# Kernel optimization log

Hardware: AMD Instinct MI355X
Metric: run time of the kernel (lower is better)

The kernel has to match this reference:

```python
import jax, jax.numpy as jnp
import numpy as np

N_CHEM = 200000
N_GENE = 20000
N_EDGES = 1000000
IN, HID, OUT = 128, 256, 128


def _seg_mean(msg, dst, num_segments):
    # DGL fn.mean: mean of incoming messages; nodes with zero in-degree get 0.
    s = jax.ops.segment_sum(msg, dst, num_segments=num_segments)
    cnt = jax.ops.segment_sum(jnp.ones((msg.shape[0],), msg.dtype), dst,
                              num_segments=num_segments)[:, None]
    return jnp.where(cnt > 0, s / jnp.maximum(cnt, 1.0), 0.0)


def setup_inputs() -> dict:
    key = jax.random.key(0)
    ks = jax.random.split(key, 12)
    d = {
        'src_cg': jax.random.randint(ks[0], (N_EDGES,), 0, N_CHEM, dtype=jnp.int32),
        'dst_cg': jax.random.randint(ks[1], (N_EDGES,), 0, N_GENE, dtype=jnp.int32),
        'src_gc': jax.random.randint(ks[2], (N_EDGES,), 0, N_GENE, dtype=jnp.int32),
        'dst_gc': jax.random.randint(ks[3], (N_EDGES,), 0, N_CHEM, dtype=jnp.int32),
        'embed_chem': jax.random.normal(ks[4], (N_CHEM, IN), jnp.float32) * 0.1,
        'embed_gene': jax.random.normal(ks[5], (N_GENE, IN), jnp.float32) * 0.1,
        'W1_cg': jax.random.normal(ks[6], (IN, HID), jnp.float32) * (1.0 / np.sqrt(IN)),
        'b1_cg': jnp.zeros((HID,), jnp.float32),
        'W1_gc': jax.random.normal(ks[7], (IN, HID), jnp.float32) * (1.0 / np.sqrt(IN)),
        'b1_gc': jnp.zeros((HID,), jnp.float32),
        'W2_cg': jax.random.normal(ks[8], (HID, OUT), jnp.float32) * (1.0 / np.sqrt(HID)),
        'b2_cg': jnp.zeros((OUT,), jnp.float32),
        'W2_gc': jax.random.normal(ks[9], (HID, OUT), jnp.float32) * (1.0 / np.sqrt(HID)),
        'b2_gc': jnp.zeros((OUT,), jnp.float32),
    }
    return d


def _layer(h_chem, h_gene, W_cg, b_cg, W_gc, b_gc, src_cg, dst_cg, src_gc, dst_gc):
    # per-etype linear transform on source features
    Wh_cg = h_chem @ W_cg + b_cg   # [N_CHEM, D]
    Wh_gc = h_gene @ W_gc + b_gc   # [N_GENE, D]
    # copy_u + mean per etype; multi_update_all('sum') -> single etype per dst here
    new_gene = _seg_mean(Wh_cg[src_cg], dst_cg, N_GENE)
    new_chem = _seg_mean(Wh_gc[src_gc], dst_gc, N_CHEM)
    return new_chem, new_gene


def reference(src_cg, dst_cg, src_gc, dst_gc, embed_chem, embed_gene,
              W1_cg, b1_cg, W1_gc, b1_gc, W2_cg, b2_cg, W2_gc, b2_gc):
    h_chem, h_gene = _layer(embed_chem, embed_gene, W1_cg, b1_cg, W1_gc, b1_gc,
                            src_cg, dst_cg, src_gc, dst_gc)
    h_chem = jax.nn.leaky_relu(h_chem, negative_slope=0.01)
    h_gene = jax.nn.leaky_relu(h_gene, negative_slope=0.01)
    h_chem, _ = _layer(h_chem, h_gene, W2_cg, b2_cg, W2_gc, b2_gc,
                       src_cg, dst_cg, src_gc, dst_gc)
    return h_chem  # [N_CHEM, OUT]
```

## Files before the change

### kernel.cpp

```cpp
#include <hip/hip_runtime.h>
#include <stdint.h>
#include <stddef.h>

#define N_CHEM 200000
#define N_GENE 20000
#define N_EDGES 1000000
#define IN_D 128
#define HID_D 256
#define OUT_D 128
#define N_SEG (N_GENE + N_CHEM)

#define NGB 313
#define NCB 391
#define NB  (NGB + NCB)
#define EPB 4096
#define NBA ((2 * N_EDGES + EPB - 1) / EPB)
#define CAP 8192
#define DROPPED 0x80000000

typedef float nfloat4 __attribute__((ext_vector_type(4)));
typedef __attribute__((ext_vector_type(8))) short bf16x8;
typedef __attribute__((ext_vector_type(4))) float f32x4;

__device__ inline unsigned bf16rne(float x) {
    unsigned u = __float_as_uint(x);
    return (u + 0x7FFFu + ((u >> 16) & 1u)) >> 16;
}

__device__ inline int bucket_of(int slot) {
    return (slot < N_GENE) ? (slot >> 6) : (NGB + ((slot - N_GENE) >> 9));
}
__device__ inline int bucket_slot0(int b) {
    return (b < NGB) ? (b << 6) : (N_GENE + ((b - NGB) << 9));
}


__global__ __launch_bounds__(256) void place_convert_kernel(
        const int* __restrict__ src_cg, const int* __restrict__ dst_cg,
        const int* __restrict__ src_gc, const int* __restrict__ dst_gc,
        int* __restrict__ bcur, unsigned* __restrict__ records,
        const float* __restrict__ conv_in, unsigned short* __restrict__ conv_out) {
    if ((int)blockIdx.x >= NBA) {
        int cb = blockIdx.x - NBA;
        const int tid = threadIdx.x;
        #pragma unroll
        for (int q = 0; q < 4; ++q) {
            int i = cb * 1024 + q * 256 + tid;
            if (i < N_CHEM * IN_D / 4) {
                float4 v = *(const float4*)&conv_in[(size_t)i * 4];
                uint2 w;
                w.x = bf16rne(v.x) | (bf16rne(v.y) << 16);
                w.y = bf16rne(v.z) | (bf16rne(v.w) << 16);
                *(uint2*)&conv_out[(size_t)i * 4] = w;
            }
        }
        return;
    }
    __shared__ unsigned stage_rec[EPB];
    __shared__ unsigned short stage_bkt[EPB];
    __shared__ int hist[NB];
    __shared__ int cursor[NB];
    __shared__ int tsum[256];
    const int tid = threadIdx.x;
    const int e0 = blockIdx.x * EPB;
    const int cnt_blk = min(EPB, 2 * N_EDGES - e0);

    for (int i = tid; i < NB; i += 256) hist[i] = 0;
    __syncthreads();

    int slotR[EPB / 256], srcR[EPB / 256];
    #pragma unroll
    for (int q = 0; q < EPB / 256; ++q) {
        int e = e0 + q * 256 + tid;
        int slot = -1, s = 0;
        if (e < N_EDGES)            { slot = dst_cg[e];                    s = src_cg[e]; }
        else if (e < 2 * N_EDGES)   { slot = N_GENE + dst_gc[e - N_EDGES]; s = src_gc[e - N_EDGES]; }
        slotR[q] = slot; srcR[q] = s;
        if (slot >= 0) atomicAdd(&hist[bucket_of(slot)], 1);
    }
    __syncthreads();

    const int b3 = tid * 3;
    int h0 = (b3     < NB) ? hist[b3]     : 0;
    int h1 = (b3 + 1 < NB) ? hist[b3 + 1] : 0;
    int h2 = (b3 + 2 < NB) ? hist[b3 + 2] : 0;
    int ts = h0 + h1 + h2;
    tsum[tid] = ts;
    __syncthreads();
    for (int off = 1; off < 256; off <<= 1) {
        int t = (tid >= off) ? tsum[tid - off] : 0;
        __syncthreads();
        tsum[tid] += t;
        __syncthreads();
    }
    int base = tsum[tid] - ts;
    if (b3     < NB) cursor[b3]     = base;
    if (b3 + 1 < NB) cursor[b3 + 1] = base + h0;
    if (b3 + 2 < NB) cursor[b3 + 2] = base + h0 + h1;
    __syncthreads();

    #pragma unroll
    for (int q = 0; q < EPB / 256; ++q) {
        int slot = slotR[q];
        if (slot >= 0) {
            int b = bucket_of(slot);
            int p = atomicAdd(&cursor[b], 1);
            stage_rec[p] = ((unsigned)(slot - bucket_slot0(b)) << 18) | (unsigned)srcR[q];
            stage_bkt[p] = (unsigned short)b;
        }
    }
    __syncthreads();

    for (int i = tid; i < NB; i += 256) {
        int n = hist[i];
        if (n) {
            int got = atomicAdd(&bcur[i], n);
            int excl_i = cursor[i] - n;
            hist[i] = (got + n <= CAP) ? (i * CAP + got - excl_i) : (int)DROPPED;
        }
    }
    __syncthreads();

    for (int i = tid; i < cnt_blk; i += 256) {
        int d = hist[stage_bkt[i]];
        if (d != (int)DROPPED) records[i + d] = stage_rec[i];
    }
}


__global__ void bucket_scan_kernel(const int* __restrict__ bcur,
                                   int* __restrict__ bbase, int* __restrict__ indptr) {
    __shared__ int sm[1024];
    const int tid = threadIdx.x;
    int v = (tid < NB) ? min(bcur[tid], CAP) : 0;
    sm[tid] = v;
    __syncthreads();
    for (int off = 1; off < 1024; off <<= 1) {
        int t = (tid >= off) ? sm[tid - off] : 0;
        __syncthreads();
        sm[tid] += t;
        __syncthreads();
    }
    if (tid < NB) bbase[tid] = sm[tid] - v;
    if (tid == NB - 1) {
        bbase[NB] = sm[tid];
        indptr[N_SEG] = sm[tid];
    }
}


__global__ __launch_bounds__(256) void bin_b_kernel(
        const unsigned* __restrict__ records, const int* __restrict__ bbase,
        const int* __restrict__ bcur,
        int* __restrict__ indptr, int* __restrict__ esrc) {
    __shared__ int hist[512];
    __shared__ int tsum[256];
    const int tid = threadIdx.x;
    const int b = blockIdx.x;
    int slot0 = bucket_slot0(b);
    int nslots = (b < NGB) ? min(64, N_GENE - slot0) : min(512, N_SEG - slot0);
    const int rbase = bbase[b];
    const int E = min(bcur[b], CAP);
    const unsigned* rec = &records[(size_t)b * CAP];

    hist[tid] = 0; hist[tid + 256] = 0;
    __syncthreads();
    for (int i = tid; i < E; i += 256)
        atomicAdd(&hist[rec[i] >> 18], 1);
    __syncthreads();

    int h0 = hist[2 * tid], h1 = hist[2 * tid + 1];
    int ts = h0 + h1;
    tsum[tid] = ts;
    __syncthreads();
    for (int off = 1; off < 256; off <<= 1) {
        int t = (tid >= off) ? tsum[tid - off] : 0;
        __syncthreads();
        tsum[tid] += t;
        __syncthreads();
    }
    int ex = tsum[tid] - ts;
    __syncthreads();
    hist[2 * tid]     = ex;
    hist[2 * tid + 1] = ex + h0;
    if (2 * tid     < nslots) indptr[slot0 + 2 * tid]     = rbase + ex;
    if (2 * tid + 1 < nslots) indptr[slot0 + 2 * tid + 1] = rbase + ex + h0;
    __syncthreads();

    for (int i = tid; i < E; i += 256) {
        unsigned r = rec[i];
        int p = atomicAdd(&hist[r >> 18], 1);
        esrc[rbase + p] = (int)(r & 0x3FFFFu);
    }
}


__device__ inline void acc_u(float* a, uint4 v) {
    a[0] += __uint_as_float(v.x << 16); a[1] += __uint_as_float(v.x & 0xffff0000u);
    a[2] += __uint_as_float(v.y << 16); a[3] += __uint_as_float(v.y & 0xffff0000u);
    a[4] += __uint_as_float(v.z << 16); a[5] += __uint_as_float(v.z & 0xffff0000u);
    a[6] += __uint_as_float(v.w << 16); a[7] += __uint_as_float(v.w & 0xffff0000u);
}


__global__ __launch_bounds__(256) void gather_mean_bf16_split_kernel(
        const unsigned short* __restrict__ table,
        const int* __restrict__ indptr, const int* __restrict__ esrc,
        unsigned short* __restrict__ outb, int n) {
    int lane = threadIdx.x & 15;
    int half = (threadIdx.x >> 4) & 1;
    int node = blockIdx.x * 8 + (threadIdx.x >> 5);
    if (node >= n) return;
    int s = indptr[node], e = indptr[node + 1];
    int deg = e - s;
    int mid = s + ((deg + 1) >> 1);
    int j0 = half ? mid : s;
    int j1 = half ? e   : mid;
    int c = lane << 3;
    float acc[8] = {};
    int j = j0;
    for (; j + 8 <= j1; j += 8) {
        int i0 = esrc[j],     i1 = esrc[j + 1], i2 = esrc[j + 2], i3 = esrc[j + 3];
        int i4 = esrc[j + 4], i5 = esrc[j + 5], i6 = esrc[j + 6], i7 = esrc[j + 7];
        uint4 v0 = *(const uint4*)&table[(size_t)i0 * 128 + c];
        uint4 v1 = *(const uint4*)&table[(size_t)i1 * 128 + c];
        uint4 v2 = *(const uint4*)&table[(size_t)i2 * 128 + c];
        uint4 v3 = *(const uint4*)&table[(size_t)i3 * 128 + c];
        uint4 v4 = *(const uint4*)&table[(size_t)i4 * 128 + c];
        uint4 v5 = *(const uint4*)&table[(size_t)i5 * 128 + c];
        uint4 v6 = *(const uint4*)&table[(size_t)i6 * 128 + c];
        uint4 v7 = *(const uint4*)&table[(size_t)i7 * 128 + c];
        acc_u(acc, v0); acc_u(acc, v1); acc_u(acc, v2); acc_u(acc, v3);
        acc_u(acc, v4); acc_u(acc, v5); acc_u(acc, v6); acc_u(acc, v7);
    }
    for (; j + 4 <= j1; j += 4) {
        uint4 v0 = *(const uint4*)&table[(size_t)esrc[j]     * 128 + c];
        uint4 v1 = *(const uint4*)&table[(size_t)esrc[j + 1] * 128 + c];
        uint4 v2 = *(const uint4*)&table[(size_t)esrc[j + 2] * 128 + c];
        uint4 v3 = *(const uint4*)&table[(size_t)esrc[j + 3] * 128 + c];
        acc_u(acc, v0); acc_u(acc, v1); acc_u(acc, v2); acc_u(acc, v3);
    }
    for (; j < j1; ++j) {
        uint4 v = *(const uint4*)&table[(size_t)esrc[j] * 128 + c];
        acc_u(acc, v);
    }
    #pragma unroll
    for (int q = 0; q < 8; ++q) acc[q] += __shfl_xor(acc[q], 16);
    if (half == 0) {
        float inv = (deg > 0) ? 1.f / (float)deg : 0.f;
        #pragma unroll
        for (int q = 0; q < 8; ++q) acc[q] *= inv;
        uint4 w;
        w.x = bf16rne(acc[0]) | (bf16rne(acc[1]) << 16);
        w.y = bf16rne(acc[2]) | (bf16rne(acc[3]) << 16);
        w.z = bf16rne(acc[4]) | (bf16rne(acc[5]) << 16);
        w.w = bf16rne(acc[6]) | (bf16rne(acc[7]) << 16);
        *(uint4*)&outb[(size_t)node * 128 + c] = w;
    }
}


template<bool NT>
__global__ __launch_bounds__(256) void gather_mean_bf16_kernel(
        const unsigned short* __restrict__ table,
        const int* __restrict__ indptr, const int* __restrict__ esrc,
        float* __restrict__ out, int n) {
    int lane = threadIdx.x & 15;
    int node = blockIdx.x * 16 + (threadIdx.x >> 4);
    if (node >= n) return;
    int s = indptr[node], e = indptr[node + 1];
    int c = lane << 3;
    float acc[8] = {};
    int j = s;
    for (; j + 4 <= e; j += 4) {
        uint4 v0 = *(const uint4*)&table[(size_t)esrc[j]     * 128 + c];
        uint4 v1 = *(const uint4*)&table[(size_t)esrc[j + 1] * 128 + c];
        uint4 v2 = *(const uint4*)&table[(size_t)esrc[j + 2] * 128 + c];
        uint4 v3 = *(const uint4*)&table[(size_t)esrc[j + 3] * 128 + c];
        acc_u(acc, v0); acc_u(acc, v1); acc_u(acc, v2); acc_u(acc, v3);
    }
    for (; j < e; ++j) {
        uint4 v = *(const uint4*)&table[(size_t)esrc[j] * 128 + c];
        acc_u(acc, v);
    }
    int deg = e - s;
    float inv = (deg > 0) ? 1.f / (float)deg : 0.f;
    #pragma unroll
    for (int q = 0; q < 8; ++q) acc[q] *= inv;
    float* dst = &out[(size_t)node * 128 + c];
    if (NT) {
        nfloat4 a = { acc[0], acc[1], acc[2], acc[3] };
        nfloat4 b = { acc[4], acc[5], acc[6], acc[7] };
        __builtin_nontemporal_store(a, (nfloat4*)dst);
        __builtin_nontemporal_store(b, (nfloat4*)(dst + 4));
    } else {
        *(float4*)dst       = make_float4(acc[0], acc[1], acc[2], acc[3]);
        *(float4*)(dst + 4) = make_float4(acc[4], acc[5], acc[6], acc[7]);
    }
}


__global__ __launch_bounds__(256) void gather_mean_f32_kernel(
        const float* __restrict__ table,
        const int* __restrict__ indptr, const int* __restrict__ esrc,
        float* __restrict__ out, int n) {
    int lane = threadIdx.x & 31;
    int node = blockIdx.x * 8 + (threadIdx.x >> 5);
    if (node >= n) return;
    int s = indptr[node], e = indptr[node + 1];
    int c = lane << 2;
    float4 acc = make_float4(0.f, 0.f, 0.f, 0.f);
    int j = s;
    for (; j + 4 <= e; j += 4) {
        int s0 = esrc[j], s1 = esrc[j + 1], s2 = esrc[j + 2], s3 = esrc[j + 3];
        float4 v0 = *(const float4*)&table[(size_t)s0 * 128 + c];
        float4 v1 = *(const float4*)&table[(size_t)s1 * 128 + c];
        float4 v2 = *(const float4*)&table[(size_t)s2 * 128 + c];
        float4 v3 = *(const float4*)&table[(size_t)s3 * 128 + c];
        acc.x += (v0.x + v1.x) + (v2.x + v3.x);
        acc.y += (v0.y + v1.y) + (v2.y + v3.y);
        acc.z += (v0.z + v1.z) + (v2.z + v3.z);
        acc.w += (v0.w + v1.w) + (v2.w + v3.w);
    }
    for (; j < e; ++j) {
        float4 v = *(const float4*)&table[(size_t)esrc[j] * 128 + c];
        acc.x += v.x; acc.y += v.y; acc.z += v.z; acc.w += v.w;
    }
    int deg = e - s;
    float inv = (deg > 0) ? 1.f / (float)deg : 0.f;
    acc.x *= inv; acc.y *= inv; acc.z *= inv; acc.w *= inv;
    *(float4*)&out[(size_t)node * 128 + c] = acc;
}


template<int K, int N, bool MASK_LEAKY>
__global__ __launch_bounds__(256) void gemm_mfma_kernel(
        const unsigned short* __restrict__ A,
        const float* __restrict__ W,
        const float* __restrict__ bias,
        const int* __restrict__ indptr,
        unsigned short* __restrict__ C,
        int M) {
    constexpr int BK  = 128;
    constexpr int LDK = BK + 8;
    __shared__ unsigned short As[64 * LDK];
    __shared__ unsigned short Ws[64 * LDK];
    const int tid  = threadIdx.x;
    const int lane = tid & 63;
    const int w    = tid >> 6;
    const int m0 = blockIdx.x * 64;
    const int n0 = blockIdx.y * 64;
    const int l15 = lane & 15;
    const int lhi = lane >> 4;
    f32x4 acc[4] = {};

    for (int kt0 = 0; kt0 < K; kt0 += BK) {
        #pragma unroll
        for (int it = 0; it < 4; ++it) {
            int idx = it * 256 + tid;
            int row = idx >> 4;
            int c8  = (idx & 15) << 3;
            uint4 v = make_uint4(0u, 0u, 0u, 0u);
            if (m0 + row < M)
                v = *(const uint4*)&A[(size_t)(m0 + row) * K + kt0 + c8];
            *(uint4*)&As[row * LDK + c8] = v;
        }
        #pragma unroll
        for (int it = 0; it < 32; ++it) {
            int i = it * 256 + tid;
            int k = i >> 6;
            int n = i & 63;
            float f = W[(size_t)(kt0 + k) * N + n0 + n];
            Ws[n * LDK + k] = (unsigned short)bf16rne(f);
        }
        __syncthreads();

        #pragma unroll
        for (int kk = 0; kk < BK; kk += 32) {
            bf16x8 a = *(const bf16x8*)&As[(w * 16 + l15) * LDK + kk + lhi * 8];
            #pragma unroll
            for (int nt = 0; nt < 4; ++nt) {
                bf16x8 b = *(const bf16x8*)&Ws[(nt * 16 + l15) * LDK + kk + lhi * 8];
                acc[nt] = __builtin_amdgcn_mfma_f32_16x16x32_bf16(a, b, acc[nt], 0, 0, 0);
            }
        }
        __syncthreads();
    }

    #pragma unroll
    for (int nt = 0; nt < 4; ++nt) {
        int col = n0 + nt * 16 + l15;
        float bz = bias[col];
        #pragma unroll
        for (int r = 0; r < 4; ++r) {
            int row = m0 + w * 16 + lhi * 4 + r;
            if (row < M) {
                float v = acc[nt][r] + bz;
                if (MASK_LEAKY) {
                    int deg = indptr[row + 1] - indptr[row];
                    v = (deg == 0) ? 0.f : (v > 0.f ? v : 0.01f * v);
                }
                C[(size_t)row * N + col] = (unsigned short)bf16rne(v);
            }
        }
    }
}


template<int K, int N, bool MASK_LEAKY, bool BF16_OUT>
__global__ __launch_bounds__(256) void gemm_kernel(const float* __restrict__ A,
                                                   const float* __restrict__ W,
                                                   const float* __restrict__ bias,
                                                   const int* __restrict__ indptr,
                                                   void* __restrict__ Cout, int M) {
    __shared__ float As[64 * 68];
    __shared__ float Ws[64 * 64];
    const int tid = threadIdx.x;
    const int tx = tid & 15, ty = tid >> 4;
    const int m0 = blockIdx.x * 64;
    const int n0 = blockIdx.y * 64;
    const int r0 = ty << 2, c0 = tx << 2;
    float acc[4][4] = {};

    for (int kt = 0; kt < K; kt += 64) {
        #pragma unroll
        for (int q = 0; q < 4; ++q) {
            int idx = tid + q * 256;
            int row = idx >> 4;
            int c4  = (idx & 15) << 2;
            float4 v = make_float4(0.f, 0.f, 0.f, 0.f);
            if (m0 + row < M)
                v = *(const float4*)&A[(size_t)(m0 + row) * K + kt + c4];
            *(float4*)&As[row * 68 + c4] = v;
        }
        #pragma unroll
        for (int q = 0; q < 4; ++q) {
            int idx = tid + q * 256;
            int k   = idx >> 4;
            int c4  = (idx & 15) << 2;
            *(float4*)&Ws[(k << 6) + c4] =
                *(const float4*)&W[(size_t)(kt + k) * N + n0 + c4];
        }
        __syncthreads();

        #pragma unroll 4
        for (int k = 0; k < 64; k += 4) {
            float a[4][4];
            #pragma unroll
            for (int r = 0; r < 4; ++r) {
                float4 v = *(const float4*)&As[(r0 + r) * 68 + k];
                a[r][0] = v.x; a[r][1] = v.y; a[r][2] = v.z; a[r][3] = v.w;
            }
            #pragma unroll
            for (int kk = 0; kk < 4; ++kk) {
                float4 w = *(const float4*)&Ws[((k + kk) << 6) + c0];
                #pragma unroll
                for (int r = 0; r < 4; ++r) {
                    acc[r][0] = fmaf(a[r][kk], w.x, acc[r][0]);
                    acc[r][1] = fmaf(a[r][kk], w.y, acc[r][1]);
                    acc[r][2] = fmaf(a[r][kk], w.z, acc[r][2]);
                    acc[r][3] = fmaf(a[r][kk], w.w, acc[r][3]);
                }
            }
        }
        __syncthreads();
    }

    float4 b = *(const float4*)&bias[n0 + c0];
    #pragma unroll
    for (int r = 0; r < 4; ++r) {
        int row = m0 + r0 + r;
        if (row < M) {
            float4 v;
            v.x = acc[r][0] + b.x; v.y = acc[r][1] + b.y;
            v.z = acc[r][2] + b.z; v.w = acc[r][3] + b.w;
            if (MASK_LEAKY) {
                int deg = indptr[row + 1] - indptr[row];
                if (deg == 0) {
                    v = make_float4(0.f, 0.f, 0.f, 0.f);
                } else {
                    v.x = v.x > 0.f ? v.x : 0.01f * v.x;
                    v.y = v.y > 0.f ? v.y : 0.01f * v.y;
                    v.z = v.z > 0.f ? v.z : 0.01f * v.z;
                    v.w = v.w > 0.f ? v.w : 0.01f * v.w;
                }
            }
            if (BF16_OUT) {
                uint2 w;
                w.x = bf16rne(v.x) | (bf16rne(v.y) << 16);
                w.y = bf16rne(v.z) | (bf16rne(v.w) << 16);
                *(uint2*)&((unsigned short*)Cout)[(size_t)row * N + n0 + c0] = w;
            } else {
                *(float4*)&((float*)Cout)[(size_t)row * N + n0 + c0] = v;
            }
        }
    }
}


extern "C" void kernel_launch(void* const* d_in, const int* in_sizes, int n_in,
                              void* d_out, int out_size, void* d_ws, size_t ws_size,
                              hipStream_t stream) {
    const int*   src_cg     = (const int*)d_in[0];
    const int*   dst_cg     = (const int*)d_in[1];
    const int*   src_gc     = (const int*)d_in[2];
    const int*   dst_gc     = (const int*)d_in[3];
    const float* embed_chem = (const float*)d_in[4];
    const float* W1_cg = (const float*)d_in[6];
    const float* b1_cg = (const float*)d_in[7];
    const float* W2_gc = (const float*)d_in[12];
    const float* b2_gc = (const float*)d_in[13];
    float* out = (float*)d_out;

    int* ws_i = (int*)d_ws;
    size_t off = 0;
    int* bcur  = ws_i + off; off += NB;
    int* bbase = ws_i + off; off += NB + 1;
    off = (off + 3) & ~(size_t)3;
    int* indptr = ws_i + off; off += N_SEG + 1; off = (off + 3) & ~(size_t)3;
    int* esrc   = ws_i + off; off += 2 * N_EDGES;
    size_t union_off = off;
    unsigned* records = (unsigned*)(ws_i + union_off);
    unsigned short* agg1b   = (unsigned short*)(ws_i + union_off);
    unsigned short* h_geneb = agg1b + (size_t)N_GENE * IN_D;
    float* agg1f   = (float*)(ws_i + union_off);
    float* h_genef = agg1f + (size_t)N_GENE * IN_D;
    size_t union_sz = (size_t)N_GENE * (IN_D + HID_D);
    off = union_off + union_sz;
    unsigned short* Wh2b = (unsigned short*)(ws_i + off); off += (size_t)N_GENE * OUT_D / 2;
    unsigned short* embedb = (unsigned short*)(ws_i + off);
    size_t off_full = off + (size_t)N_CHEM * IN_D / 2;
    const bool bf16_embed = ws_size >= off_full * sizeof(int);

    (void)hipMemsetAsync(bcur, 0, NB * sizeof(int), stream);

    const int nconv = bf16_embed ? (N_CHEM * IN_D / 4 + 1023) / 1024 : 0;
    place_convert_kernel<<<NBA + nconv, 256, 0, stream>>>(
        src_cg, dst_cg, src_gc, dst_gc, bcur, records, embed_chem, embedb);
    bucket_scan_kernel<<<1, 1024, 0, stream>>>(bcur, bbase, indptr);
    bin_b_kernel<<<NB, 256, 0, stream>>>(records, bbase, bcur, indptr, esrc);

    if (bf16_embed) {
        gather_mean_bf16_split_kernel<<<(N_GENE + 7) / 8, 256, 0, stream>>>(
            embedb, indptr, esrc, agg1b, N_GENE);
        {
            dim3 g((N_GENE + 63) / 64, HID_D / 64), blk(256);
            gemm_mfma_kernel<IN_D, HID_D, true><<<g, blk, 0, stream>>>(
                agg1b, W1_cg, b1_cg, indptr, h_geneb, N_GENE);
        }
        {
            dim3 g((N_GENE + 63) / 64, OUT_D / 64), blk(256);
            gemm_mfma_kernel<HID_D, OUT_D, false><<<g, blk, 0, stream>>>(
                h_geneb, W2_gc, b2_gc, nullptr, Wh2b, N_GENE);
        }
    } else {
        gather_mean_f32_kernel<<<(N_GENE + 7) / 8, 256, 0, stream>>>(
            embed_chem, indptr, esrc, agg1f, N_GENE);
        {
            dim3 g((N_GENE + 63) / 64, HID_D / 64), blk(256);
            gemm_kernel<IN_D, HID_D, true, false><<<g, blk, 0, stream>>>(
                agg1f, W1_cg, b1_cg, indptr, h_genef, N_GENE);
        }
        {
            dim3 g((N_GENE + 63) / 64, OUT_D / 64), blk(256);
            gemm_kernel<HID_D, OUT_D, false, true><<<g, blk, 0, stream>>>(
                h_genef, W2_gc, b2_gc, nullptr, Wh2b, N_GENE);
        }
    }

    gather_mean_bf16_kernel<true><<<(N_CHEM + 15) / 16, 256, 0, stream>>>(
        Wh2b, indptr + N_GENE, esrc, out, N_CHEM);
}
```

Before: 378.0 us.

## Drop bucket scan via fixed-capacity CSR and fuse the two gene GEMMs

Removes the single-block bucket scan kernel by giving each bucket a fixed CAP-sized region of esrc and storing per-node start/end arrays instead of a compact indptr. It also fuses the layer-1 GEMM (with bias, degree mask and leaky ReLU) and the layer-2 GEMM into one kernel that keeps the 64x256 hidden tile in shared memory as bf16. This saves two kernel launches plus the global write and read of the hidden activations. In exchange, esrc becomes a larger sparse buffer, the workspace grows, and the fused kernel uses more LDS per block and launches only a 1D grid of row tiles, which lowers parallelism.

Measured after the change: 380.9 us. No clear change (+0.8%).

```diff
diff --git a/kernel.cpp b/kernel.cpp
--- a/kernel.cpp
+++ b/kernel.cpp
@@ -128,38 +128,16 @@
 }
 
 
-__global__ void bucket_scan_kernel(const int* __restrict__ bcur,
-                                   int* __restrict__ bbase, int* __restrict__ indptr) {
-    __shared__ int sm[1024];
-    const int tid = threadIdx.x;
-    int v = (tid < NB) ? min(bcur[tid], CAP) : 0;
-    sm[tid] = v;
-    __syncthreads();
-    for (int off = 1; off < 1024; off <<= 1) {
-        int t = (tid >= off) ? sm[tid - off] : 0;
-        __syncthreads();
-        sm[tid] += t;
-        __syncthreads();
-    }
-    if (tid < NB) bbase[tid] = sm[tid] - v;
-    if (tid == NB - 1) {
-        bbase[NB] = sm[tid];
-        indptr[N_SEG] = sm[tid];
-    }
-}
-
-
 __global__ __launch_bounds__(256) void bin_b_kernel(
-        const unsigned* __restrict__ records, const int* __restrict__ bbase,
-        const int* __restrict__ bcur,
-        int* __restrict__ indptr, int* __restrict__ esrc) {
+        const unsigned* __restrict__ records, const int* __restrict__ bcur,
+        int* __restrict__ istart, int* __restrict__ iend, int* __restrict__ esrc) {
     __shared__ int hist[512];
     __shared__ int tsum[256];
     const int tid = threadIdx.x;
     const int b = blockIdx.x;
     int slot0 = bucket_slot0(b);
     int nslots = (b < NGB) ? min(64, N_GENE - slot0) : min(512, N_SEG - slot0);
-    const int rbase = bbase[b];
+    const int rbase = b * CAP;
     const int E = min(bcur[b], CAP);
     const unsigned* rec = &records[(size_t)b * CAP];
 
@@ -183,8 +161,14 @@
     __syncthreads();
     hist[2 * tid]     = ex;
     hist[2 * tid + 1] = ex + h0;
-    if (2 * tid     < nslots) indptr[slot0 + 2 * tid]     = rbase + ex;
-    if (2 * tid + 1 < nslots) indptr[slot0 + 2 * tid + 1] = rbase + ex + h0;
+    if (2 * tid < nslots) {
+        istart[slot0 + 2 * tid] = rbase + ex;
+        iend[slot0 + 2 * tid]   = rbase + ex + h0;
+    }
+    if (2 * tid + 1 < nslots) {
+        istart[slot0 + 2 * tid + 1] = rbase + ex + h0;
+        iend[slot0 + 2 * tid + 1]   = rbase + ex + h0 + h1;
+    }
     __syncthreads();
 
     for (int i = tid; i < E; i += 256) {
@@ -205,13 +189,14 @@
 
 __global__ __launch_bounds__(256) void gather_mean_bf16_split_kernel(
         const unsigned short* __restrict__ table,
-        const int* __restrict__ indptr, const int* __restrict__ esrc,
+        const int* __restrict__ istart, const int* __restrict__ iend,
+        const int* __restrict__ esrc,
         unsigned short* __restrict__ outb, int n) {
     int lane = threadIdx.x & 15;
     int half = (threadIdx.x >> 4) & 1;
     int node = blockIdx.x * 8 + (threadIdx.x >> 5);
     if (node >= n) return;
-    int s = indptr[node], e = indptr[node + 1];
+    int s = istart[node], e = iend[node];
     int deg = e - s;
     int mid = s + ((deg + 1) >> 1);
     int j0 = half ? mid : s;
@@ -263,12 +248,13 @@
 template<bool NT>
 __global__ __launch_bounds__(256) void gather_mean_bf16_kernel(
         const unsigned short* __restrict__ table,
-        const int* __restrict__ indptr, const int* __restrict__ esrc,
+        const int* __restrict__ istart, const int* __restrict__ iend,
+        const int* __restrict__ esrc,
         float* __restrict__ out, int n) {
     int lane = threadIdx.x & 15;
     int node = blockIdx.x * 16 + (threadIdx.x >> 4);
     if (node >= n) return;
-    int s = indptr[node], e = indptr[node + 1];
+    int s = istart[node], e = iend[node];
     int c = lane << 3;
     float acc[8] = {};
     int j = s;
@@ -302,12 +288,13 @@
 
 __global__ __launch_bounds__(256) void gather_mean_f32_kernel(
         const float* __restrict__ table,
-        const int* __restrict__ indptr, const int* __restrict__ esrc,
+        const int* __restrict__ istart, const int* __restrict__ iend,
+        const int* __restrict__ esrc,
         float* __restrict__ out, int n) {
     int lane = threadIdx.x & 31;
     int node = blockIdx.x * 8 + (threadIdx.x >> 5);
     if (node >= n) return;
-    int s = indptr[node], e = indptr[node + 1];
+    int s = istart[node], e = iend[node];
     int c = lane << 2;
     float4 acc = make_float4(0.f, 0.f, 0.f, 0.f);
     int j = s;
@@ -333,50 +320,51 @@
 }
 
 
-template<int K, int N, bool MASK_LEAKY>
-__global__ __launch_bounds__(256) void gemm_mfma_kernel(
+__global__ __launch_bounds__(256) void gemm_fused_kernel(
         const unsigned short* __restrict__ A,
-        const float* __restrict__ W,
-        const float* __restrict__ bias,
-        const int* __restrict__ indptr,
+        const float* __restrict__ W1,
+        const float* __restrict__ b1,
+        const float* __restrict__ W2,
+        const float* __restrict__ b2,
+        const int* __restrict__ istart, const int* __restrict__ iend,
         unsigned short* __restrict__ C,
         int M) {
-    constexpr int BK  = 128;
-    constexpr int LDK = BK + 8;
-    __shared__ unsigned short As[64 * LDK];
-    __shared__ unsigned short Ws[64 * LDK];
+    constexpr int LDK = 136;
+    constexpr int LDH = 264;
+    __shared__ unsigned short SAB[2 * 64 * LDK];
+    __shared__ unsigned short Ht[64 * LDH];
+    unsigned short* As = SAB;
+    unsigned short* Ws = SAB + 64 * LDK;
     const int tid  = threadIdx.x;
     const int lane = tid & 63;
     const int w    = tid >> 6;
-    const int m0 = blockIdx.x * 64;
-    const int n0 = blockIdx.y * 64;
-    const int l15 = lane & 15;
-    const int lhi = lane >> 4;
-    f32x4 acc[4] = {};
-
-    for (int kt0 = 0; kt0 < K; kt0 += BK) {
-        #pragma unroll
-        for (int it = 0; it < 4; ++it) {
-            int idx = it * 256 + tid;
-            int row = idx >> 4;
-            int c8  = (idx & 15) << 3;
-            uint4 v = make_uint4(0u, 0u, 0u, 0u);
-            if (m0 + row < M)
-                v = *(const uint4*)&A[(size_t)(m0 + row) * K + kt0 + c8];
-            *(uint4*)&As[row * LDK + c8] = v;
-        }
+    const int m0   = blockIdx.x * 64;
+    const int l15  = lane & 15;
+    const int lhi  = lane >> 4;
+
+    #pragma unroll
+    for (int it = 0; it < 4; ++it) {
+        int idx = it * 256 + tid;
+        int row = idx >> 4;
+        int c8  = (idx & 15) << 3;
+        uint4 v = make_uint4(0u, 0u, 0u, 0u);
+        if (m0 + row < M)
+            v = *(const uint4*)&A[(size_t)(m0 + row) * IN_D + c8];
+        *(uint4*)&As[row * LDK + c8] = v;
+    }
+    for (int n0c = 0; n0c < HID_D; n0c += 64) {
+        __syncthreads();
         #pragma unroll
         for (int it = 0; it < 32; ++it) {
             int i = it * 256 + tid;
             int k = i >> 6;
             int n = i & 63;
-            float f = W[(size_t)(kt0 + k) * N + n0 + n];
-            Ws[n * LDK + k] = (unsigned short)bf16rne(f);
-        }
-        __syncthreads();
-
-        #pragma unroll
-        for (int kk = 0; kk < BK; kk += 32) {
+            Ws[n * LDK + k] = (unsigned short)bf16rne(W1[(size_t)k * HID_D + n0c + n]);
+        }
+        __syncthreads();
+        f32x4 acc[4] = {};
+        #pragma unroll
+        for (int kk = 0; kk < 128; kk += 32) {
             bf16x8 a = *(const bf16x8*)&As[(w * 16 + l15) * LDK + kk + lhi * 8];
             #pragma unroll
             for (int nt = 0; nt < 4; ++nt) {
@@ -384,23 +372,55 @@
                 acc[nt] = __builtin_amdgcn_mfma_f32_16x16x32_bf16(a, b, acc[nt], 0, 0, 0);
             }
         }
-        __syncthreads();
-    }
-
-    #pragma unroll
-    for (int nt = 0; nt < 4; ++nt) {
-        int col = n0 + nt * 16 + l15;
-        float bz = bias[col];
+        #pragma unroll
+        for (int nt = 0; nt < 4; ++nt) {
+            int col = n0c + nt * 16 + l15;
+            float bz = b1[col];
+            #pragma unroll
+            for (int r = 0; r < 4; ++r) {
+                int row = w * 16 + lhi * 4 + r;
+                if (m0 + row < M) {
+                    float v = acc[nt][r] + bz;
+                    int deg = iend[m0 + row] - istart[m0 + row];
+                    v = (deg == 0) ? 0.f : (v > 0.f ? v : 0.01f * v);
+                    Ht[row * LDH + col] = (unsigned short)bf16rne(v);
+                }
+            }
+        }
+    }
+    __syncthreads();
+
+    f32x4 acc2[8] = {};
+    for (int kt = 0; kt < HID_D; kt += 128) {
+        #pragma unroll
+        for (int it = 0; it < 64; ++it) {
+            int i = it * 256 + tid;
+            int k = i >> 7;
+            int n = i & 127;
+            SAB[n * LDK + k] = (unsigned short)bf16rne(W2[(size_t)(kt + k) * OUT_D + n]);
+        }
+        __syncthreads();
+        #pragma unroll
+        for (int kk = 0; kk < 128; kk += 32) {
+            bf16x8 a = *(const bf16x8*)&Ht[(w * 16 + l15) * LDH + kt + kk + lhi * 8];
+            #pragma unroll
+            for (int nt = 0; nt < 8; ++nt) {
+                bf16x8 b = *(const bf16x8*)&SAB[(nt * 16 + l15) * LDK + kk + lhi * 8];
+                acc2[nt] = __builtin_amdgcn_mfma_f32_16x16x32_bf16(a, b, acc2[nt], 0, 0, 0);
+            }
+        }
+        __syncthreads();
+    }
+    #pragma unroll
+    for (int nt = 0; nt < 8; ++nt) {
+        int col = nt * 16 + l15;
+        float bz = b2[col];
         #pragma unroll
         for (int r = 0; r < 4; ++r) {
             int row = m0 + w * 16 + lhi * 4 + r;
             if (row < M) {
-                float v = acc[nt][r] + bz;
-                if (MASK_LEAKY) {
-                    int deg = indptr[row + 1] - indptr[row];
-                    v = (deg == 0) ? 0.f : (v > 0.f ? v : 0.01f * v);
-                }
-                C[(size_t)row * N + col] = (unsigned short)bf16rne(v);
+                float v = acc2[nt][r] + bz;
+                C[(size_t)row * OUT_D + col] = (unsigned short)bf16rne(v);
             }
         }
     }
@@ -411,7 +431,8 @@
 __global__ __launch_bounds__(256) void gemm_kernel(const float* __restrict__ A,
                                                    const float* __restrict__ W,
                                                    const float* __restrict__ bias,
-                                                   const int* __restrict__ indptr,
+                                                   const int* __restrict__ istart,
+                                                   const int* __restrict__ iend,
                                                    void* __restrict__ Cout, int M) {
     __shared__ float As[64 * 68];
     __shared__ float Ws[64 * 64];
@@ -475,7 +496,7 @@
             v.x = acc[r][0] + b.x; v.y = acc[r][1] + b.y;
             v.z = acc[r][2] + b.z; v.w = acc[r][3] + b.w;
             if (MASK_LEAKY) {
-                int deg = indptr[row + 1] - indptr[row];
+                int deg = iend[row] - istart[row];
                 if (deg == 0) {
                     v = make_float4(0.f, 0.f, 0.f, 0.f);
                 } else {
@@ -514,18 +535,18 @@
 
     int* ws_i = (int*)d_ws;
     size_t off = 0;
-    int* bcur  = ws_i + off; off += NB;
-    int* bbase = ws_i + off; off += NB + 1;
+    int* bcur   = ws_i + off; off += NB;
+    int* istart = ws_i + off; off += N_SEG;
+    int* iend   = ws_i + off; off += N_SEG;
     off = (off + 3) & ~(size_t)3;
-    int* indptr = ws_i + off; off += N_SEG + 1; off = (off + 3) & ~(size_t)3;
-    int* esrc   = ws_i + off; off += 2 * N_EDGES;
+    int* esrc   = ws_i + off; off += (size_t)NB * CAP;
     size_t union_off = off;
     unsigned* records = (unsigned*)(ws_i + union_off);
-    unsigned short* agg1b   = (unsigned short*)(ws_i + union_off);
-    unsigned short* h_geneb = agg1b + (size_t)N_GENE * IN_D;
+    unsigned short* agg1b = (unsigned short*)(ws_i + union_off);
     float* agg1f   = (float*)(ws_i + union_off);
     float* h_genef = agg1f + (size_t)N_GENE * IN_D;
-    size_t union_sz = (size_t)N_GENE * (IN_D + HID_D);
+    size_t union_sz = (size_t)NB * CAP;
+    if (union_sz < (size_t)N_GENE * (IN_D + HID_D)) union_sz = (size_t)N_GENE * (IN_D + HID_D);
     off = union_off + union_sz;
     unsigned short* Wh2b = (unsigned short*)(ws_i + off); off += (size_t)N_GENE * OUT_D / 2;
     unsigned short* embedb = (unsigned short*)(ws_i + off);
@@ -537,37 +558,28 @@
     const int nconv = bf16_embed ? (N_CHEM * IN_D / 4 + 1023) / 1024 : 0;
     place_convert_kernel<<<NBA + nconv, 256, 0, stream>>>(
         src_cg, dst_cg, src_gc, dst_gc, bcur, records, embed_chem, embedb);
-    bucket_scan_kernel<<<1, 1024, 0, stream>>>(bcur, bbase, indptr);
-    bin_b_kernel<<<NB, 256, 0, stream>>>(records, bbase, bcur, indptr, esrc);
+    bin_b_kernel<<<NB, 256, 0, stream>>>(records, bcur, istart, iend, esrc);
 
     if (bf16_embed) {
         gather_mean_bf16_split_kernel<<<(N_GENE + 7) / 8, 256, 0, stream>>>(
-            embedb, indptr, esrc, agg1b, N_GENE);
-        {
-            dim3 g((N_GENE + 63) / 64, HID_D / 64), blk(256);
-            gemm_mfma_kernel<IN_D, HID_D, true><<<g, blk, 0, stream>>>(
-                agg1b, W1_cg, b1_cg, indptr, h_geneb, N_GENE);
-        }
-        {
-            dim3 g((N_GENE + 63) / 64, OUT_D / 64), blk(256);
-            gemm_mfma_kernel<HID_D, OUT_D, false><<<g, blk, 0, stream>>>(
-                h_geneb, W2_gc, b2_gc, nullptr, Wh2b, N_GENE);
-        }
+            embedb, istart, iend, esrc, agg1b, N_GENE);
+        gemm_fused_kernel<<<(N_GENE + 63) / 64, 256, 0, stream>>>(
+            agg1b, W1_cg, b1_cg, W2_gc, b2_gc, istart, iend, Wh2b, N_GENE);
     } else {
         gather_mean_f32_kernel<<<(N_GENE + 7) / 8, 256, 0, stream>>>(
-            embed_chem, indptr, esrc, agg1f, N_GENE);
+            embed_chem, istart, iend, esrc, agg1f, N_GENE);
         {
             dim3 g((N_GENE + 63) / 64, HID_D / 64), blk(256);
             gemm_kernel<IN_D, HID_D, true, false><<<g, blk, 0, stream>>>(
-                agg1f, W1_cg, b1_cg, indptr, h_genef, N_GENE);
+                agg1f, W1_cg, b1_cg, istart, iend, h_genef, N_GENE);
         }
         {
             dim3 g((N_GENE + 63) / 64, OUT_D / 64), blk(256);
             gemm_kernel<HID_D, OUT_D, false, true><<<g, blk, 0, stream>>>(
-                h_genef, W2_gc, b2_gc, nullptr, Wh2b, N_GENE);
+                h_genef, W2_gc, b2_gc, istart, iend, Wh2b, N_GENE);
         }
     }
 
     gather_mean_bf16_kernel<true><<<(N_CHEM + 15) / 16, 256, 0, stream>>>(
-        Wh2b, indptr + N_GENE, esrc, out, N_CHEM);
-}
+        Wh2b, istart + N_GENE, iend + N_GENE, esrc, out, N_CHEM);
+}
```
